# Kernel tuning notes

Measured on AMD Instinct MI355X. Metric: run time of the kernel, lower is better.

## Reference

```python
import jax, jax.numpy as jnp
import numpy as np

BS, NE, NN, CIN, H, D = 8, 4800, 4981, 3, 128, 6
EPG = 19200
NEDGE = BS * EPG
N = BS * NE

PARAM_NAMES = [
    'enc_cw1','enc_cb1','enc_cw2','enc_cb2','enc_cw3','enc_clng','enc_clnb',
    'enc_ew1','enc_eb1','enc_ew2','enc_eb2','enc_ew3','enc_elng','enc_elnb',
    'p_ew1','p_eb1','p_ew2','p_eb2','p_ew3','p_elng','p_elnb',
    'p_nw1','p_nb1','p_nw2','p_nb2','p_nw3','p_nlng','p_nlnb',
    'dec_uw1','dec_ub1','dec_uw2','dec_ub2','dec_uw3','dec_ulng','dec_ulnb',
    'dec_cw1','dec_cb1','dec_cw2','dec_cb2','dec_cw3']


def setup_inputs():
    key = jax.random.key(0)
    ks = iter(jax.random.split(key, 64))
    def nrm(shape, s=0.1):
        return jax.random.normal(next(ks), shape, jnp.float32) * s
    inp = {}
    inp['x'] = jax.random.normal(next(ks), (BS * NN, CIN), jnp.float32)
    inp['elem_conn'] = jax.random.randint(next(ks), (NE, 4), 0, NN)
    inp['edge_index'] = jax.random.randint(next(ks), (2, NEDGE), 0, N)
    inp['enc_cw1'] = nrm((CIN, 4, 1)); inp['enc_cb1'] = nrm((CIN, 1), 0.01)
    inp['enc_cw2'] = nrm((CIN, 1, 1)); inp['enc_cb2'] = nrm((CIN, 1), 0.01)
    inp['enc_cw3'] = nrm((CIN, 1, 1))
    inp['enc_clng'] = jnp.ones((CIN, 1)); inp['enc_clnb'] = jnp.zeros((CIN, 1))
    inp['enc_ew1'] = nrm((CIN, H)); inp['enc_eb1'] = nrm((H,), 0.01)
    inp['enc_ew2'] = nrm((H, H)); inp['enc_eb2'] = nrm((H,), 0.01)
    inp['enc_ew3'] = nrm((H, H))
    inp['enc_elng'] = jnp.ones((H,)); inp['enc_elnb'] = jnp.zeros((H,))
    inp['p_ew1'] = nrm((D, 2 * H, H)); inp['p_eb1'] = nrm((D, H), 0.01)
    inp['p_ew2'] = nrm((D, H, H)); inp['p_eb2'] = nrm((D, H), 0.01)
    inp['p_ew3'] = nrm((D, H, H))
    inp['p_elng'] = jnp.ones((D, H)); inp['p_elnb'] = jnp.zeros((D, H))
    inp['p_nw1'] = nrm((D, 2 * H, H)); inp['p_nb1'] = nrm((D, H), 0.01)
    inp['p_nw2'] = nrm((D, H, H)); inp['p_nb2'] = nrm((D, H), 0.01)
    inp['p_nw3'] = nrm((D, H, H))
    inp['p_nlng'] = jnp.ones((D, H)); inp['p_nlnb'] = jnp.zeros((D, H))
    inp['dec_uw1'] = nrm((H, 1, 4)); inp['dec_ub1'] = nrm((H, 4), 0.01)
    inp['dec_uw2'] = nrm((H, 4, 4)); inp['dec_ub2'] = nrm((H, 4), 0.01)
    inp['dec_uw3'] = nrm((H, 4, 4))
    inp['dec_ulng'] = jnp.ones((H, 4)); inp['dec_ulnb'] = jnp.zeros((H, 4))
    inp['dec_cw1'] = nrm((H, CIN)); inp['dec_cb1'] = nrm((CIN,), 0.01)
    inp['dec_cw2'] = nrm((CIN, CIN)); inp['dec_cb2'] = nrm((CIN,), 0.01)
    inp['dec_cw3'] = nrm((CIN, CIN))
    return inp


def lrelu(x):
    return jnp.where(x >= 0, x, 0.2 * x)


def ln(x, g, b, axis=-1):
    m = jnp.mean(x, axis=axis, keepdims=True)
    v = jnp.var(x, axis=axis, keepdims=True)
    return (x - m) / jnp.sqrt(v + 1e-5) * g + b


def mlp(x, w1, b1, w2, b2, w3):
    h = lrelu(x @ w1 + b1)
    h = lrelu(h @ w2 + b2)
    return h @ w3


def _forward(fl, elem_conn, edge_index):
    x = fl[0]
    P = dict(zip(PARAM_NAMES, fl[1:]))
    # ---- Encoder: MeshCNN gather (4 mesh nodes per element) + per-channel MLP 4->1 ----
    xg = x.reshape(BS, NN, CIN)[:, elem_conn]                  # (BS, NE, 4, CIN)
    h = lrelu(jnp.einsum('beic,cio->beoc', xg, P['enc_cw1']) + P['enc_cb1'].T[None, None])
    h = lrelu(jnp.einsum('beic,cio->beoc', h, P['enc_cw2']) + P['enc_cb2'].T[None, None])
    h = jnp.einsum('beic,cio->beoc', h, P['enc_cw3'])
    h = ln(h, P['enc_clng'].T[None, None], P['enc_clnb'].T[None, None], axis=2)  # LayerNorm(1)
    h = h[:, :, 0, :].reshape(N, CIN)
    h = ln(mlp(h, P['enc_ew1'], P['enc_eb1'], P['enc_ew2'], P['enc_eb2'], P['enc_ew3']),
           P['enc_elng'], P['enc_elnb'])                       # (N, H)
    # ---- Processor: D GraphNet blocks, edge MLP + scatter-add + node MLP ----
    src, dest = edge_index[0], edge_index[1]
    stacked = (P['p_ew1'], P['p_eb1'], P['p_ew2'], P['p_eb2'], P['p_ew3'], P['p_elng'], P['p_elnb'],
               P['p_nw1'], P['p_nb1'], P['p_nw2'], P['p_nb2'], P['p_nw3'], P['p_nlng'], P['p_nlnb'])
    def step(hc, p):
        ew1, eb1, ew2, eb2, ew3, eg, ebv, nw1, nb1, nw2, nb2, nw3, ng, nbv = p
        msg = jnp.concatenate([hc[dest], hc[src]], axis=-1)    # (NEDGE, 2H)
        m = ln(mlp(msg, ew1, eb1, ew2, eb2, ew3), eg, ebv)
        aggr = jax.ops.segment_sum(m, dest, num_segments=N)
        hn = ln(mlp(jnp.concatenate([hc, aggr], axis=-1), nw1, nb1, nw2, nb2, nw3), ng, nbv)
        return hn, None
    h, _ = jax.lax.scan(step, h, stacked)
    # ---- Decoder: per-channel upsample 1->4 then index_add back to mesh nodes ----
    u = h.reshape(BS, NE, H)[:, :, None, :]                    # (BS, NE, 1, H)
    u = lrelu(jnp.einsum('beic,cio->beoc', u, P['dec_uw1']) + P['dec_ub1'].T[None, None])
    u = lrelu(jnp.einsum('beic,cio->beoc', u, P['dec_uw2']) + P['dec_ub2'].T[None, None])
    u = jnp.einsum('beic,cio->beoc', u, P['dec_uw3'])
    u = ln(u, P['dec_ulng'].T[None, None], P['dec_ulnb'].T[None, None], axis=2)  # (BS, NE, 4, H)
    out = jnp.zeros((BS, NN, H), u.dtype).at[:, elem_conn.reshape(-1)].add(u.reshape(BS, NE * 4, H))
    out = out.reshape(BS * NN, H)
    o = lrelu(out @ P['dec_cw1'] + P['dec_cb1'])
    o = lrelu(o @ P['dec_cw2'] + P['dec_cb2'])
    return o @ P['dec_cw3']


def reference(x, elem_conn, edge_index,
              enc_cw1, enc_cb1, enc_cw2, enc_cb2, enc_cw3, enc_clng, enc_clnb,
              enc_ew1, enc_eb1, enc_ew2, enc_eb2, enc_ew3, enc_elng, enc_elnb,
              p_ew1, p_eb1, p_ew2, p_eb2, p_ew3, p_elng, p_elnb,
              p_nw1, p_nb1, p_nw2, p_nb2, p_nw3, p_nlng, p_nlnb,
              dec_uw1, dec_ub1, dec_uw2, dec_ub2, dec_uw3, dec_ulng, dec_ulnb,
              dec_cw1, dec_cb1, dec_cw2, dec_cb2, dec_cw3):
    fl = (x, enc_cw1, enc_cb1, enc_cw2, enc_cb2, enc_cw3, enc_clng, enc_clnb,
          enc_ew1, enc_eb1, enc_ew2, enc_eb2, enc_ew3, enc_elng, enc_elnb,
          p_ew1, p_eb1, p_ew2, p_eb2, p_ew3, p_elng, p_elnb,
          p_nw1, p_nb1, p_nw2, p_nb2, p_nw3, p_nlng, p_nlnb,
          dec_uw1, dec_ub1, dec_uw2, dec_ub2, dec_uw3, dec_ulng, dec_ulnb,
          dec_cw1, dec_cb1, dec_cw2, dec_cb2, dec_cw3)
    return _forward(fl, elem_conn, edge_index)
```

## Files before the change

kernel.cpp:

```cpp
#include <hip/hip_runtime.h>
#include <hip/hip_fp16.h>
#include <math.h>

#define BS    8
#define NE    4800
#define NN    4981
#define CIN   3
#define HD    128
#define DBLK  6
#define NEDGE 153600
#define NTOT  38400
#define NMESH (BS*NN)
#define NNP   5120
#define EM    128
#define TROWS 256

#define UW1T  0
#define UB1T  512
#define UW2T  1024
#define UB2T  3072
#define UW3T  3584
#define ULNGT 5632
#define ULNBT 6144
#define DWT_N 6656

typedef _Float16 f16;
typedef _Float16 f16x8 __attribute__((ext_vector_type(8)));
typedef float f32x4 __attribute__((ext_vector_type(4)));

__device__ __forceinline__ float lrelu(float x) { return x >= 0.0f ? x : 0.2f * x; }

__global__ __launch_bounds__(128)
void enc_msg0_kernel(const float* __restrict__ clnb,
                     const float* __restrict__ ew1, const float* __restrict__ eb1,
                     const float* __restrict__ ew2, const float* __restrict__ eb2,
                     const float* __restrict__ ew3,
                     const float* __restrict__ g, const float* __restrict__ b,
                     float* __restrict__ hv0,
                     const float* __restrict__ pew1, const float* __restrict__ peb1,
                     const float* __restrict__ pew2, const float* __restrict__ peb2,
                     const float* __restrict__ pew3,
                     const float* __restrict__ pg, const float* __restrict__ pb,
                     float* __restrict__ m0) {
    __shared__ float s1[HD], s2[HD], s3[HD], hv[HD];
    int j = threadIdx.x;
    float a = eb1[j];
    for (int c = 0; c < CIN; ++c) a += clnb[c] * ew1[c * HD + j];
    s1[j] = lrelu(a);
    __syncthreads();
    a = eb2[j];
    for (int k = 0; k < HD; ++k) a += s1[k] * ew2[k * HD + j];
    s2[j] = lrelu(a);
    __syncthreads();
    a = 0.0f;
    for (int k = 0; k < HD; ++k) a += s2[k] * ew3[k * HD + j];
    s3[j] = a;
    __syncthreads();
    float m = 0.0f;
    for (int k = 0; k < HD; ++k) m += s3[k];
    m *= (1.0f / HD);
    float v = 0.0f;
    for (int k = 0; k < HD; ++k) { float d = s3[k] - m; v += d * d; }
    v *= (1.0f / HD);
    float rs = 1.0f / sqrtf(v + 1e-5f);
    float h0 = (s3[j] - m) * rs * g[j] + b[j];
    hv0[j] = h0;
    hv[j] = h0;
    __syncthreads();
    a = peb1[j];
    for (int k = 0; k < HD; ++k) a += hv[k] * (pew1[k * HD + j] + pew1[(k + HD) * HD + j]);
    s1[j] = lrelu(a);
    __syncthreads();
    a = peb2[j];
    for (int k = 0; k < HD; ++k) a += s1[k] * pew2[k * HD + j];
    s2[j] = lrelu(a);
    __syncthreads();
    a = 0.0f;
    for (int k = 0; k < HD; ++k) a += s2[k] * pew3[k * HD + j];
    s3[j] = a;
    __syncthreads();
    m = 0.0f;
    for (int k = 0; k < HD; ++k) m += s3[k];
    m *= (1.0f / HD);
    v = 0.0f;
    for (int k = 0; k < HD; ++k) { float d = s3[k] - m; v += d * d; }
    v *= (1.0f / HD);
    rs = 1.0f / sqrtf(v + 1e-5f);
    m0[j] = (s3[j] - m) * rs * pg[j] + pb[j];
}

__global__ __launch_bounds__(256)
void conv_all_kernel(const float* __restrict__ ew1, const float* __restrict__ ew2,
                     const float* __restrict__ ew3,
                     const float* __restrict__ nw1, const float* __restrict__ nw2,
                     const float* __restrict__ nw3, f16* __restrict__ wbuf,
                     const float* __restrict__ eb1, f16* __restrict__ eb16,
                     const float* __restrict__ uw1, const float* __restrict__ ub1,
                     const float* __restrict__ uw2, const float* __restrict__ ub2,
                     const float* __restrict__ uw3, const float* __restrict__ ulng,
                     const float* __restrict__ ulnb, float* __restrict__ dwt,
                     int* __restrict__ degIota) {
    int b = blockIdx.x;
    int tid = threadIdx.x;
    if (b == 48) {
        for (int i = tid; i < DBLK * HD; i += 256)
            eb16[i] = (f16)eb1[i];
        degIota[tid] = tid;
        return;
    }
    if (b == 49) {
        for (int idx = tid; idx < 512; idx += 256) {
            int o = idx >> 7, c = idx & 127;
            dwt[UW1T + idx] = uw1[c * 4 + o];
            dwt[UB1T + idx] = ub1[c * 4 + o];
            dwt[UB2T + idx] = ub2[c * 4 + o];
            dwt[ULNGT + idx] = ulng[c * 4 + o];
            dwt[ULNBT + idx] = ulnb[c * 4 + o];
        }
        for (int idx = tid; idx < 2048; idx += 256) {
            int io = idx >> 7, c = idx & 127;
            dwt[UW2T + idx] = uw2[c * 16 + io];
            dwt[UW3T + idx] = uw3[c * 16 + io];
        }
        return;
    }
    int d = b >> 3, m = b & 7;
    const float* src;
    switch (m) {
        case 0: src = ew1 + (size_t)d * 2 * HD * HD; break;
        case 1: src = ew1 + (size_t)d * 2 * HD * HD + HD * HD; break;
        case 2: src = ew2 + (size_t)d * HD * HD; break;
        case 3: src = ew3 + (size_t)d * HD * HD; break;
        case 4: src = nw1 + (size_t)d * 2 * HD * HD; break;
        case 5: src = nw1 + (size_t)d * 2 * HD * HD + HD * HD; break;
        case 6: src = nw2 + (size_t)d * HD * HD; break;
        default: src = nw3 + (size_t)d * HD * HD; break;
    }
    f16* out = wbuf + (size_t)b * HD * HD;
    for (int idx = tid; idx < HD * HD; idx += 256) {
        int n = idx >> 7, k = idx & 127;
        out[idx] = (f16)src[k * HD + n];
    }
}

#define EHB (NEDGE / 256)
#define MHB (NE * 4 / 256)
#define ESB (NTOT / 256)
#define MSB (NNP / 256)

__global__ __launch_bounds__(256)
void prep_hist(const int* __restrict__ e_dst, const int* __restrict__ conn,
               int* __restrict__ deg, int* __restrict__ mdeg) {
    int b = blockIdx.x;
    if (b < EHB) {
        int e = b * 256 + threadIdx.x;
        atomicAdd(&deg[e_dst[e]], 1);
    } else {
        int idx = (b - EHB) * 256 + threadIdx.x;
        atomicAdd(&mdeg[conn[idx]], 1);
    }
}

__device__ __forceinline__ void scan1_body(const int* __restrict__ deg,
                                           int* __restrict__ rowptr,
                                           int* __restrict__ bsum, int bi) {
    __shared__ int s[256];
    int i = bi * 256 + threadIdx.x;
    int v = deg[i];
    s[threadIdx.x] = v;
    __syncthreads();
    for (int off = 1; off < 256; off <<= 1) {
        int t = (threadIdx.x >= off) ? s[threadIdx.x - off] : 0;
        __syncthreads();
        s[threadIdx.x] += t;
        __syncthreads();
    }
    rowptr[i] = s[threadIdx.x] - v;
    if (threadIdx.x == 255) bsum[bi] = s[255];
}

__global__ __launch_bounds__(256)
void prep_scan1(const int* __restrict__ deg, int* __restrict__ rowptr,
                int* __restrict__ bsum,
                const int* __restrict__ mdeg, int* __restrict__ mrow,
                int* __restrict__ mbsum) {
    int b = blockIdx.x;
    if (b < ESB) scan1_body(deg, rowptr, bsum, b);
    else         scan1_body(mdeg, mrow, mbsum, b - ESB);
}

__device__ __forceinline__ void scan2_body(int* __restrict__ bsum, int nb) {
    __shared__ int s[256];
    int v = (threadIdx.x < nb) ? bsum[threadIdx.x] : 0;
    s[threadIdx.x] = v;
    __syncthreads();
    for (int off = 1; off < 256; off <<= 1) {
        int t = (threadIdx.x >= off) ? s[threadIdx.x - off] : 0;
        __syncthreads();
        s[threadIdx.x] += t;
        __syncthreads();
    }
    if (threadIdx.x < nb) bsum[threadIdx.x] = s[threadIdx.x] - v;
}

__global__ __launch_bounds__(256)
void prep_scan2(int* __restrict__ bsum, int* __restrict__ mbsum) {
    if (blockIdx.x == 0) scan2_body(bsum, ESB);
    else                 scan2_body(mbsum, MSB);
}

__global__ __launch_bounds__(256)
void prep_scan3(int* __restrict__ rowptr, const int* __restrict__ bsum,
                int* __restrict__ mrow, const int* __restrict__ mbsum) {
    int b = blockIdx.x;
    if (b < ESB) {
        int i = b * 256 + threadIdx.x;
        rowptr[i] += bsum[b];
    } else {
        int i = (b - ESB) * 256 + threadIdx.x;
        mrow[i] += mbsum[b - ESB];
    }
}

__global__ __launch_bounds__(256)
void prep_scatter(const int* __restrict__ dest, const int* __restrict__ srcv,
                  const int* __restrict__ rowptr, int* __restrict__ cursor,
                  int* __restrict__ dsorted, int* __restrict__ ssorted,
                  const int* __restrict__ conn, const int* __restrict__ mrow,
                  int* __restrict__ mcur, int* __restrict__ mslot,
                  const int* __restrict__ deg,
                  int* __restrict__ ddegs, int* __restrict__ sdegs) {
    int b = blockIdx.x;
    if (b < EHB) {
        int e = b * 256 + threadIdx.x;
        int d = dest[e];
        int s = srcv[e];
        int pos = rowptr[d] + atomicAdd(&cursor[d], 1);
        dsorted[pos] = d;
        ssorted[pos] = s;
        ddegs[pos] = deg[d];
        sdegs[pos] = deg[s];
    } else {
        int idx = (b - EHB) * 256 + threadIdx.x;
        int nd = conn[idx];
        int pos = mrow[nd] + atomicAdd(&mcur[nd], 1);
        mslot[pos] = idx;
    }
}

template <int NT>
__device__ __forceinline__ void stage_w(const f16* __restrict__ Wg, f16 (*Bt)[HD + 8],
                                        int tid) {
    #pragma unroll
    for (int t = 0; t < 2048 / NT; ++t) {
        int idx = tid + t * NT;
        int r = idx >> 4, c = (idx & 15) * 8;
        *(uint4*)(&Bt[r][c]) = *(const uint4*)(Wg + (size_t)r * HD + c);
    }
}

__device__ __forceinline__ void mfma_pass(const f16 (*A)[HD + 8], const f16 (*Bt)[HD + 8],
                                          int rt_base, int ct_base, int ln, int quad,
                                          f32x4 acc[2][4]) {
    #pragma unroll
    for (int ks = 0; ks < 4; ++ks) {
        int kb = ks * 32 + quad * 8;
        f16x8 a0 = *(const f16x8*)(&A[rt_base + ln][kb]);
        f16x8 a1 = *(const f16x8*)(&A[rt_base + 16 + ln][kb]);
        #pragma unroll
        for (int c = 0; c < 4; ++c) {
            f16x8 b = *(const f16x8*)(&Bt[ct_base + c * 16 + ln][kb]);
            acc[0][c] = __builtin_amdgcn_mfma_f32_16x16x32_f16(a0, b, acc[0][c], 0, 0, 0);
            acc[1][c] = __builtin_amdgcn_mfma_f32_16x16x32_f16(a1, b, acc[1][c], 0, 0, 0);
        }
    }
}

__global__ __launch_bounds__(512, 4)
void gn_edge(const f16* __restrict__ P1, const f16* __restrict__ P2,
             const int* __restrict__ dsorted, const int* __restrict__ ssorted,
             const f16* __restrict__ W2, const f16* __restrict__ W3,
             const f16* __restrict__ b1h, const float* __restrict__ b2,
             const float* __restrict__ g, const float* __restrict__ bln,
             f16* __restrict__ msg) {
    __shared__ __align__(16) f16 As[EM][HD + 8];
    __shared__ __align__(16) f16 Bt[HD][HD + 8];
    __shared__ float red[EM][2][2];

    const int tid = threadIdx.x;
    const int base = blockIdx.x * EM;
    const int wave = tid >> 6, lane = tid & 63;
    const int ln = lane & 15, quad = lane >> 4;
    const int rt_base = (wave >> 1) * 32;
    const int ct_base = (wave & 1) * 64;
    const int half = wave & 1;
    const int r0 = tid >> 4;
    const int cg = (tid & 15) * 8;

    const f16 k02s = (f16)0.2f;
    const f16x8 k02 = {k02s, k02s, k02s, k02s, k02s, k02s, k02s, k02s};

    int dI[4], sI[4];
    #pragma unroll
    for (int it = 0; it < 4; ++it) {
        dI[it] = dsorted[base + r0 + it * 32];
        sI[it] = ssorted[base + r0 + it * 32];
    }
    stage_w<512>(W2, Bt, tid);
    const f16x8 bb = *(const f16x8*)(b1h + cg);
    #pragma unroll
    for (int it = 0; it < 4; ++it) {
        f16x8 p1 = *(const f16x8*)(P1 + (size_t)dI[it] * HD + cg);
        f16x8 p2 = *(const f16x8*)(P2 + (size_t)sI[it] * HD + cg);
        f16x8 s = p1 + p2 + bb;
        *(f16x8*)(&As[r0 + it * 32][cg]) = __builtin_elementwise_max(s, s * k02);
    }
    __syncthreads();

    f32x4 acc[2][4];

    #pragma unroll
    for (int c = 0; c < 4; ++c) {
        float bj = b2[ct_base + c * 16 + ln];
        f32x4 bv = {bj, bj, bj, bj};
        acc[0][c] = bv; acc[1][c] = bv;
    }
    mfma_pass(As, Bt, rt_base, ct_base, ln, quad, acc);
    __syncthreads();
    stage_w<512>(W3, Bt, tid);
    #pragma unroll
    for (int i = 0; i < 2; ++i)
        #pragma unroll
        for (int c = 0; c < 4; ++c)
            #pragma unroll
            for (int r = 0; r < 4; ++r)
                As[rt_base + i * 16 + quad * 4 + r][ct_base + c * 16 + ln] =
                    (f16)lrelu(acc[i][c][r]);
    __syncthreads();

    #pragma unroll
    for (int c = 0; c < 4; ++c) { f32x4 z = {0,0,0,0}; acc[0][c] = z; acc[1][c] = z; }
    mfma_pass(As, Bt, rt_base, ct_base, ln, quad, acc);

    #pragma unroll
    for (int i = 0; i < 2; ++i)
        #pragma unroll
        for (int r = 0; r < 4; ++r) {
            float s = acc[i][0][r] + acc[i][1][r] + acc[i][2][r] + acc[i][3][r];
            float q = acc[i][0][r] * acc[i][0][r] + acc[i][1][r] * acc[i][1][r] +
                      acc[i][2][r] * acc[i][2][r] + acc[i][3][r] * acc[i][3][r];
            s += __shfl_xor(s, 1); q += __shfl_xor(q, 1);
            s += __shfl_xor(s, 2); q += __shfl_xor(q, 2);
            s += __shfl_xor(s, 4); q += __shfl_xor(q, 4);
            s += __shfl_xor(s, 8); q += __shfl_xor(q, 8);
            if (ln == 0) {
                int row = rt_base + i * 16 + quad * 4 + r;
                red[row][half][0] = s;
                red[row][half][1] = q;
            }
        }
    __syncthreads();

    float gv[4], bv[4];
    #pragma unroll
    for (int c = 0; c < 4; ++c) {
        int col = ct_base + c * 16 + ln;
        gv[c] = g[col]; bv[c] = bln[col];
    }
    #pragma unroll
    for (int i = 0; i < 2; ++i)
        #pragma unroll
        for (int r = 0; r < 4; ++r) {
            int row = rt_base + i * 16 + quad * 4 + r;
            float s = red[row][0][0] + red[row][1][0];
            float q = red[row][0][1] + red[row][1][1];
            float m = s * (1.0f / HD);
            float var = q * (1.0f / HD) - m * m;
            float rs = 1.0f / sqrtf(var + 1e-5f);
            #pragma unroll
            for (int c = 0; c < 4; ++c) {
                int col = ct_base + c * 16 + ln;
                float v = (acc[i][c][r] - m) * rs * gv[c] + bv[c];
                msg[(size_t)(base + row) * HD + col] = (f16)v;
            }
        }
}

template <int AGGR, bool PROD, bool DECF, bool HTAB>
__global__ __launch_bounds__(256, 3)
void gn_node(f16* __restrict__ h16, const f16* __restrict__ msg,
             const int* __restrict__ rowptr, const int* __restrict__ deg,
             const float* __restrict__ m0, const float* __restrict__ hv0,
             const f16* __restrict__ htab,
             const f16* __restrict__ W1a, const f16* __restrict__ W1b,
             const f16* __restrict__ W2, const f16* __restrict__ W3,
             const float* __restrict__ b1, const float* __restrict__ b2,
             const float* __restrict__ g, const float* __restrict__ bln,
             const f16* __restrict__ nW1a, const f16* __restrict__ nW1b,
             f16* __restrict__ P1, f16* __restrict__ P2,
             const float* __restrict__ dwt, f16* __restrict__ uval) {
    __shared__ __align__(16) f16 As[64][HD + 8];
    __shared__ __align__(16) f16 Bt[HD][HD + 8];
    __shared__ float red[64][2][2];

    const int tid = threadIdx.x;
    const int base = blockIdx.x * 64;
    const int wave = tid >> 6, lane = tid & 63;
    const int ln = lane & 15, quad = lane >> 4;
    const int rt_base = (wave >> 1) * 32;
    const int ct_base = (wave & 1) * 64;
    const int half = wave & 1;

    f16x8 hreg[4];
    #pragma unroll
    for (int t = 0; t < 4; ++t) {
        int r = (tid >> 4) + t * 16;
        int c = (tid & 15) * 8;
        if (AGGR == 0) {
            f16x8 hz;
            #pragma unroll
            for (int u = 0; u < 8; ++u) hz[u] = (f16)hv0[c + u];
            hreg[t] = hz;
            float sc = (float)deg[base + r];
            f16x8 o;
            #pragma unroll
            for (int u = 0; u < 8; ++u) o[u] = (f16)(sc * m0[c + u]);
            *(f16x8*)(&As[r][c]) = o;
        } else {
            if (HTAB)
                hreg[t] = *(const f16x8*)(htab + (size_t)deg[base + r] * HD + c);
            else
                hreg[t] = *(const f16x8*)(h16 + (size_t)(base + r) * HD + c);
            int rp = rowptr[base + r], dg = deg[base + r];
            float a[8] = {0, 0, 0, 0, 0, 0, 0, 0};
            int j = 0;
            for (; j + 4 <= dg; j += 4) {
                f16x8 v0 = *(const f16x8*)(msg + (size_t)(rp + j) * HD + c);
                f16x8 v1 = *(const f16x8*)(msg + (size_t)(rp + j + 1) * HD + c);
                f16x8 v2 = *(const f16x8*)(msg + (size_t)(rp + j + 2) * HD + c);
                f16x8 v3 = *(const f16x8*)(msg + (size_t)(rp + j + 3) * HD + c);
                #pragma unroll
                for (int u = 0; u < 8; ++u)
                    a[u] += ((float)v0[u] + (float)v1[u]) + ((float)v2[u] + (float)v3[u]);
            }
            for (; j < dg; ++j) {
                f16x8 mv = *(const f16x8*)(msg + (size_t)(rp + j) * HD + c);
                #pragma unroll
                for (int u = 0; u < 8; ++u) a[u] += (float)mv[u];
            }
            f16x8 o;
            #pragma unroll
            for (int u = 0; u < 8; ++u) o[u] = (f16)a[u];
            *(f16x8*)(&As[r][c]) = o;
        }
    }
    stage_w<256>(W1b, Bt, tid);
    __syncthreads();

    f32x4 acc[2][4];
    #pragma unroll
    for (int c = 0; c < 4; ++c) {
        float bj = b1[ct_base + c * 16 + ln];
        f32x4 bb = {bj, bj, bj, bj};
        acc[0][c] = bb; acc[1][c] = bb;
    }
    mfma_pass(As, Bt, rt_base, ct_base, ln, quad, acc);
    __syncthreads();

    #pragma unroll
    for (int t = 0; t < 4; ++t) {
        int r = (tid >> 4) + t * 16;
        int c = (tid & 15) * 8;
        *(f16x8*)(&As[r][c]) = hreg[t];
    }
    stage_w<256>(W1a, Bt, tid);
    __syncthreads();
    mfma_pass(As, Bt, rt_base, ct_base, ln, quad, acc);
    __syncthreads();

    stage_w<256>(W2, Bt, tid);
    #pragma unroll
    for (int i = 0; i < 2; ++i)
        #pragma unroll
        for (int c = 0; c < 4; ++c)
            #pragma unroll
            for (int r = 0; r < 4; ++r)
                As[rt_base + i * 16 + quad * 4 + r][ct_base + c * 16 + ln] =
                    (f16)lrelu(acc[i][c][r]);
    __syncthreads();

    #pragma unroll
    for (int c = 0; c < 4; ++c) {
        float bj = b2[ct_base + c * 16 + ln];
        f32x4 bb = {bj, bj, bj, bj};
        acc[0][c] = bb; acc[1][c] = bb;
    }
    mfma_pass(As, Bt, rt_base, ct_base, ln, quad, acc);
    __syncthreads();
    stage_w<256>(W3, Bt, tid);
    #pragma unroll
    for (int i = 0; i < 2; ++i)
        #pragma unroll
        for (int c = 0; c < 4; ++c)
            #pragma unroll
            for (int r = 0; r < 4; ++r)
                As[rt_base + i * 16 + quad * 4 + r][ct_base + c * 16 + ln] =
                    (f16)lrelu(acc[i][c][r]);
    __syncthreads();

    #pragma unroll
    for (int c = 0; c < 4; ++c) { f32x4 z = {0,0,0,0}; acc[0][c] = z; acc[1][c] = z; }
    mfma_pass(As, Bt, rt_base, ct_base, ln, quad, acc);

    #pragma unroll
    for (int i = 0; i < 2; ++i)
        #pragma unroll
        for (int r = 0; r < 4; ++r) {
            float s = acc[i][0][r] + acc[i][1][r] + acc[i][2][r] + acc[i][3][r];
            float q = acc[i][0][r] * acc[i][0][r] + acc[i][1][r] * acc[i][1][r] +
                      acc[i][2][r] * acc[i][2][r] + acc[i][3][r] * acc[i][3][r];
            s += __shfl_xor(s, 1); q += __shfl_xor(q, 1);
            s += __shfl_xor(s, 2); q += __shfl_xor(q, 2);
            s += __shfl_xor(s, 4); q += __shfl_xor(q, 4);
            s += __shfl_xor(s, 8); q += __shfl_xor(q, 8);
            if (ln == 0) {
                int row = rt_base + i * 16 + quad * 4 + r;
                red[row][half][0] = s;
                red[row][half][1] = q;
            }
        }
    __syncthreads();

    float gv[4], bv[4];
    #pragma unroll
    for (int c = 0; c < 4; ++c) {
        int col = ct_base + c * 16 + ln;
        gv[c] = g[col]; bv[c] = bln[col];
    }

    if (!DECF) {
        #pragma unroll
        for (int i = 0; i < 2; ++i)
            #pragma unroll
            for (int r = 0; r < 4; ++r) {
                int row = rt_base + i * 16 + quad * 4 + r;
                float s = red[row][0][0] + red[row][1][0];
                float q = red[row][0][1] + red[row][1][1];
                float m = s * (1.0f / HD);
                float var = q * (1.0f / HD) - m * m;
                float rs = 1.0f / sqrtf(var + 1e-5f);
                #pragma unroll
                for (int c = 0; c < 4; ++c) {
                    int col = ct_base + c * 16 + ln;
                    float v = (acc[i][c][r] - m) * rs * gv[c] + bv[c];
                    f16 hv = (f16)v;
                    h16[(size_t)(base + row) * HD + col] = hv;
                    if (PROD) As[row][col] = hv;
                }
            }
    } else {
        float mm[2][4], rr[2][4];
        #pragma unroll
        for (int i = 0; i < 2; ++i)
            #pragma unroll
            for (int r = 0; r < 4; ++r) {
                int row = rt_base + i * 16 + quad * 4 + r;
                float s = red[row][0][0] + red[row][1][0];
                float q = red[row][0][1] + red[row][1][1];
                float m = s * (1.0f / HD);
                float var = q * (1.0f / HD) - m * m;
                mm[i][r] = m;
                rr[i][r] = 1.0f / sqrtf(var + 1e-5f);
            }
        #pragma unroll
        for (int c = 0; c < 4; ++c) {
            int col = ct_base + c * 16 + ln;
            float w1v[4], wb1[4], wb2[4], lg4[4], lb4[4];
            #pragma unroll
            for (int o = 0; o < 4; ++o) {
                w1v[o] = dwt[UW1T + o * 128 + col];
                wb1[o] = dwt[UB1T + o * 128 + col];
                wb2[o] = dwt[UB2T + o * 128 + col];
                lg4[o] = dwt[ULNGT + o * 128 + col];
                lb4[o] = dwt[ULNBT + o * 128 + col];
            }
            float w2v[16], w3v[16];
            #pragma unroll
            for (int io = 0; io < 16; ++io) {
                w2v[io] = dwt[UW2T + io * 128 + col];
                w3v[io] = dwt[UW3T + io * 128 + col];
            }
            #pragma unroll
            for (int i = 0; i < 2; ++i)
                #pragma unroll
                for (int r = 0; r < 4; ++r) {
                    int row = rt_base + i * 16 + quad * 4 + r;
                    float v = (acc[i][c][r] - mm[i][r]) * rr[i][r] * gv[c] + bv[c];
                    float s = (float)(f16)v;
                    float u1[4], u2[4], u3[4];
                    #pragma unroll
                    for (int o = 0; o < 4; ++o)
                        u1[o] = lrelu(s * w1v[o] + wb1[o]);
                    #pragma unroll
                    for (int o = 0; o < 4; ++o) {
                        float a = wb2[o];
                        #pragma unroll
                        for (int i2 = 0; i2 < 4; ++i2) a += u1[i2] * w2v[i2 * 4 + o];
                        u2[o] = lrelu(a);
                    }
                    #pragma unroll
                    for (int o = 0; o < 4; ++o) {
                        float a = 0.f;
                        #pragma unroll
                        for (int i2 = 0; i2 < 4; ++i2) a += u2[i2] * w3v[i2 * 4 + o];
                        u3[o] = a;
                    }
                    float m4 = 0.25f * (u3[0] + u3[1] + u3[2] + u3[3]);
                    float var4 = 0.f;
                    #pragma unroll
                    for (int o = 0; o < 4; ++o) { float d = u3[o] - m4; var4 += d * d; }
                    var4 *= 0.25f;
                    float rs4 = 1.0f / sqrtf(var4 + 1e-5f);
                    size_t ub = (size_t)(base + row) * 4 * HD + col;
                    #pragma unroll
                    for (int o = 0; o < 4; ++o)
                        uval[ub + (size_t)o * HD] =
                            (f16)((u3[o] - m4) * rs4 * lg4[o] + lb4[o]);
                }
        }
    }

    if (PROD) {
        __syncthreads();
        stage_w<256>(nW1a, Bt, tid);
        __syncthreads();
        #pragma unroll
        for (int c = 0; c < 4; ++c) { f32x4 z = {0,0,0,0}; acc[0][c] = z; acc[1][c] = z; }
        mfma_pass(As, Bt, rt_base, ct_base, ln, quad, acc);
        #pragma unroll
        for (int i = 0; i < 2; ++i)
            #pragma unroll
            for (int c = 0; c < 4; ++c)
                #pragma unroll
                for (int r = 0; r < 4; ++r)
                    P1[(size_t)(base + rt_base + i * 16 + quad * 4 + r) * HD +
                       ct_base + c * 16 + ln] = (f16)acc[i][c][r];
        __syncthreads();
        stage_w<256>(nW1b, Bt, tid);
        __syncthreads();
        #pragma unroll
        for (int c = 0; c < 4; ++c) { f32x4 z = {0,0,0,0}; acc[0][c] = z; acc[1][c] = z; }
        mfma_pass(As, Bt, rt_base, ct_base, ln, quad, acc);
        #pragma unroll
        for (int i = 0; i < 2; ++i)
            #pragma unroll
            for (int c = 0; c < 4; ++c)
                #pragma unroll
                for (int r = 0; r < 4; ++r)
                    P2[(size_t)(base + rt_base + i * 16 + quad * 4 + r) * HD +
                       ct_base + c * 16 + ln] = (f16)acc[i][c][r];
    }
}

__global__ __launch_bounds__(256)
void dec_gather_out(const f16* __restrict__ uval,
                    const int* __restrict__ mrow, const int* __restrict__ mdeg,
                    const int* __restrict__ mslot,
                    const float* __restrict__ cw1, const float* __restrict__ cb1,
                    const float* __restrict__ cw2, const float* __restrict__ cb2,
                    const float* __restrict__ cw3,
                    float* __restrict__ o, int nrows) {
    int r = blockIdx.x * 4 + (threadIdx.x >> 6);
    if (r >= nrows) return;
    int lane = threadIdx.x & 63;
    int b = r / NN, n = r - b * NN;
    int rp = mrow[n], dg = mdeg[n];
    size_t boff = (size_t)b * NE * 4;
    float a0 = 0.f, a1 = 0.f;
    int j = 0;
    for (; j + 4 <= dg; j += 4) {
        int s0 = mslot[rp + j], s1 = mslot[rp + j + 1];
        int s2 = mslot[rp + j + 2], s3 = mslot[rp + j + 3];
        const f16* u0 = uval + (boff + s0) * HD + lane * 2;
        const f16* u1 = uval + (boff + s1) * HD + lane * 2;
        const f16* u2 = uval + (boff + s2) * HD + lane * 2;
        const f16* u3 = uval + (boff + s3) * HD + lane * 2;
        float b00 = (float)u0[0], b01 = (float)u0[1];
        float b10 = (float)u1[0], b11 = (float)u1[1];
        float b20 = (float)u2[0], b21 = (float)u2[1];
        float b30 = (float)u3[0], b31 = (float)u3[1];
        a0 += (b00 + b10) + (b20 + b30);
        a1 += (b01 + b11) + (b21 + b31);
    }
    for (; j < dg; ++j) {
        int slot = mslot[rp + j];
        const f16* up = uval + (boff + slot) * HD + lane * 2;
        a0 += (float)up[0];
        a1 += (float)up[1];
    }
    int c0 = lane * 2, c1 = lane * 2 + 1;
    float s[3];
    #pragma unroll
    for (int k = 0; k < 3; ++k)
        s[k] = a0 * cw1[c0 * 3 + k] + a1 * cw1[c1 * 3 + k];
    #pragma unroll
    for (int off = 32; off >= 1; off >>= 1) {
        s[0] += __shfl_down(s[0], off);
        s[1] += __shfl_down(s[1], off);
        s[2] += __shfl_down(s[2], off);
    }
    if (lane == 0) {
        float t1[3], t2[3];
        #pragma unroll
        for (int k = 0; k < 3; ++k) t1[k] = lrelu(s[k] + cb1[k]);
        #pragma unroll
        for (int k = 0; k < 3; ++k) {
            float a = cb2[k];
            #pragma unroll
            for (int q = 0; q < 3; ++q) a += t1[q] * cw2[q * 3 + k];
            t2[k] = lrelu(a);
        }
        #pragma unroll
        for (int k = 0; k < 3; ++k) {
            float a = 0.f;
            #pragma unroll
            for (int q = 0; q < 3; ++q) a += t2[q] * cw3[q * 3 + k];
            o[(size_t)r * 3 + k] = a;
        }
    }
}

extern "C" void kernel_launch(void* const* d_in, const int* in_sizes, int n_in,
                              void* d_out, int out_size, void* d_ws, size_t ws_size,
                              hipStream_t stream) {
    const int* elem_conn = (const int*)d_in[1];
    const int* edge_index = (const int*)d_in[2];
    const int* e_src = edge_index;
    const int* e_dst = edge_index + NEDGE;
    const float* enc_clnb = (const float*)d_in[9];
    const float* enc_ew1 = (const float*)d_in[10];
    const float* enc_eb1 = (const float*)d_in[11];
    const float* enc_ew2 = (const float*)d_in[12];
    const float* enc_eb2 = (const float*)d_in[13];
    const float* enc_ew3 = (const float*)d_in[14];
    const float* enc_elng = (const float*)d_in[15];
    const float* enc_elnb = (const float*)d_in[16];
    const float* p_ew1 = (const float*)d_in[17];
    const float* p_eb1 = (const float*)d_in[18];
    const float* p_ew2 = (const float*)d_in[19];
    const float* p_eb2 = (const float*)d_in[20];
    const float* p_ew3 = (const float*)d_in[21];
    const float* p_elng = (const float*)d_in[22];
    const float* p_elnb = (const float*)d_in[23];
    const float* p_nw1 = (const float*)d_in[24];
    const float* p_nb1 = (const float*)d_in[25];
    const float* p_nw2 = (const float*)d_in[26];
    const float* p_nb2 = (const float*)d_in[27];
    const float* p_nw3 = (const float*)d_in[28];
    const float* p_nlng = (const float*)d_in[29];
    const float* p_nlnb = (const float*)d_in[30];
    const float* dec_uw1 = (const float*)d_in[31];
    const float* dec_ub1 = (const float*)d_in[32];
    const float* dec_uw2 = (const float*)d_in[33];
    const float* dec_ub2 = (const float*)d_in[34];
    const float* dec_uw3 = (const float*)d_in[35];
    const float* dec_ulng = (const float*)d_in[36];
    const float* dec_ulnb = (const float*)d_in[37];
    const float* dec_cw1 = (const float*)d_in[38];
    const float* dec_cb1 = (const float*)d_in[39];
    const float* dec_cw2 = (const float*)d_in[40];
    const float* dec_cb2 = (const float*)d_in[41];
    const float* dec_cw3 = (const float*)d_in[42];

    char* ws = (char*)d_ws;
    f16*   h16     = (f16*)(ws);
    f16*   wbuf    = (f16*)(ws + 9830400);
    float* hv0     = (float*)(ws + 11403264);
    float* m0      = (float*)(ws + 11403776);
    f16*   P1      = (f16*)(ws + 11404288);
    f16*   P2      = (f16*)(ws + 21234688);
    f16*   msg     = (f16*)(ws + 31065088);
    int*   deg     = (int*)(ws + 70386688);
    int*   rowptr  = (int*)(ws + 70540288);
    int*   cursor  = (int*)(ws + 70693888);
    int*   bsum    = (int*)(ws + 70847488);
    int*   dsorted = (int*)(ws + 70848512);
    int*   ssorted = (int*)(ws + 71462912);
    f16*   eb16    = (f16*)(ws + 72077312);
    int*   mdeg    = (int*)(ws + 72078848);
    int*   mrow    = (int*)(ws + 72099328);
    int*   mcur    = (int*)(ws + 72119808);
    int*   mbsum   = (int*)(ws + 72140288);
    int*   mslot   = (int*)(ws + 72141312);
    float* dwt     = (float*)(ws + 72218112);
    f16*   uval    = (f16*)(ws + 72244736);
    int*   ddegs   = (int*)(ws + 111566336);
    int*   sdegs   = (int*)(ws + 112180736);
    f16*   tabH    = (f16*)(ws + 112795136);
    f16*   tabP1   = (f16*)(ws + 112860672);
    f16*   tabP2   = (f16*)(ws + 112926208);
    int*   degIota = (int*)(ws + 112991744);

    hipMemsetAsync(deg, 0, 72218112 - 70386688, stream);

    enc_msg0_kernel<<<1, 128, 0, stream>>>(
        enc_clnb, enc_ew1, enc_eb1, enc_ew2, enc_eb2, enc_ew3, enc_elng, enc_elnb, hv0,
        p_ew1, p_eb1, p_ew2, p_eb2, p_ew3, p_elng, p_elnb, m0);
    conv_all_kernel<<<50, 256, 0, stream>>>(p_ew1, p_ew2, p_ew3,
                                            p_nw1, p_nw2, p_nw3, wbuf, p_eb1, eb16,
                                            dec_uw1, dec_ub1, dec_uw2, dec_ub2,
                                            dec_uw3, dec_ulng, dec_ulnb, dwt,
                                            degIota);

    {
        const f16* wd = wbuf;
        const f16* wn = wbuf + (size_t)8 * HD * HD;
        gn_node<0, true, false, false><<<TROWS / 64, 256, 0, stream>>>(
            tabH, nullptr, nullptr, degIota, m0, hv0, nullptr,
            wd + 4 * HD * HD, wd + 5 * HD * HD, wd + 6 * HD * HD, wd + 7 * HD * HD,
            p_nb1, p_nb2, p_nlng, p_nlnb,
            wn + 0 * HD * HD, wn + 1 * HD * HD, tabP1, tabP2, nullptr, nullptr);
    }

    prep_hist<<<EHB + MHB, 256, 0, stream>>>(e_dst, elem_conn, deg, mdeg);
    prep_scan1<<<ESB + MSB, 256, 0, stream>>>(deg, rowptr, bsum, mdeg, mrow, mbsum);
    prep_scan2<<<2, 256, 0, stream>>>(bsum, mbsum);
    prep_scan3<<<ESB + MSB, 256, 0, stream>>>(rowptr, bsum, mrow, mbsum);
    prep_scatter<<<EHB + MHB, 256, 0, stream>>>(e_dst, e_src, rowptr, cursor,
                                                dsorted, ssorted,
                                                elem_conn, mrow, mcur, mslot,
                                                deg, ddegs, sdegs);

    for (int d = 1; d < DBLK; ++d) {
        const f16* wd = wbuf + (size_t)d * 8 * HD * HD;
        if (d == 1)
            gn_edge<<<NEDGE / EM, 512, 0, stream>>>(
                tabP1, tabP2, ddegs, sdegs,
                wd + 2 * HD * HD, wd + 3 * HD * HD,
                eb16 + (size_t)d * HD, p_eb2 + (size_t)d * HD,
                p_elng + (size_t)d * HD, p_elnb + (size_t)d * HD, msg);
        else
            gn_edge<<<NEDGE / EM, 512, 0, stream>>>(
                P1, P2, dsorted, ssorted,
                wd + 2 * HD * HD, wd + 3 * HD * HD,
                eb16 + (size_t)d * HD, p_eb2 + (size_t)d * HD,
                p_elng + (size_t)d * HD, p_elnb + (size_t)d * HD, msg);
        if (d == 1) {
            const f16* wn = wbuf + (size_t)(d + 1) * 8 * HD * HD;
            gn_node<1, true, false, true><<<NTOT / 64, 256, 0, stream>>>(
                h16, msg, rowptr, deg, nullptr, nullptr, tabH,
                wd + 4 * HD * HD, wd + 5 * HD * HD, wd + 6 * HD * HD, wd + 7 * HD * HD,
                p_nb1 + (size_t)d * HD, p_nb2 + (size_t)d * HD,
                p_nlng + (size_t)d * HD, p_nlnb + (size_t)d * HD,
                wn + 0 * HD * HD, wn + 1 * HD * HD, P1, P2, nullptr, nullptr);
        } else if (d < DBLK - 1) {
            const f16* wn = wbuf + (size_t)(d + 1) * 8 * HD * HD;
            gn_node<1, true, false, false><<<NTOT / 64, 256, 0, stream>>>(
                h16, msg, rowptr, deg, nullptr, nullptr, nullptr,
                wd + 4 * HD * HD, wd + 5 * HD * HD, wd + 6 * HD * HD, wd + 7 * HD * HD,
                p_nb1 + (size_t)d * HD, p_nb2 + (size_t)d * HD,
                p_nlng + (size_t)d * HD, p_nlnb + (size_t)d * HD,
                wn + 0 * HD * HD, wn + 1 * HD * HD, P1, P2, nullptr, nullptr);
        } else {
            gn_node<1, false, true, false><<<NTOT / 64, 256, 0, stream>>>(
                h16, msg, rowptr, deg, nullptr, nullptr, nullptr,
                wd + 4 * HD * HD, wd + 5 * HD * HD, wd + 6 * HD * HD, wd + 7 * HD * HD,
                p_nb1 + (size_t)d * HD, p_nb2 + (size_t)d * HD,
                p_nlng + (size_t)d * HD, p_nlnb + (size_t)d * HD,
                wbuf, wbuf, P1, P2, dwt, uval);
        }
    }

    dec_gather_out<<<(NMESH + 3) / 4, 256, 0, stream>>>(
        uval, mrow, mdeg, mslot, dec_cw1, dec_cb1, dec_cw2, dec_cb2, dec_cw3,
        (float*)d_out, NMESH);
}
```

Measured before the change: 564.7 us.

## Fold memset and scan2 into other kernels, pack decoder u-values per channel

```diff
diff --git a/kernel.cpp b/kernel.cpp
--- a/kernel.cpp
+++ b/kernel.cpp
@@ -26,6 +26,7 @@
 
 typedef _Float16 f16;
 typedef _Float16 f16x8 __attribute__((ext_vector_type(8)));
+typedef _Float16 f16x4 __attribute__((ext_vector_type(4)));
 typedef float f32x4 __attribute__((ext_vector_type(4)));
 
 __device__ __forceinline__ float lrelu(float x) { return x >= 0.0f ? x : 0.2f * x; }
@@ -99,7 +100,9 @@
                      const float* __restrict__ uw2, const float* __restrict__ ub2,
                      const float* __restrict__ uw3, const float* __restrict__ ulng,
                      const float* __restrict__ ulnb, float* __restrict__ dwt,
-                     int* __restrict__ degIota) {
+                     int* __restrict__ degIota,
+                     int* __restrict__ zdeg, int* __restrict__ zcur,
+                     int* __restrict__ zmdeg, int* __restrict__ zmcur) {
     int b = blockIdx.x;
     int tid = threadIdx.x;
     if (b == 48) {
@@ -121,6 +124,16 @@
             int io = idx >> 7, c = idx & 127;
             dwt[UW2T + idx] = uw2[c * 16 + io];
             dwt[UW3T + idx] = uw3[c * 16 + io];
+        }
+        return;
+    }
+    if (b >= 50) {
+        uint4 z = {0, 0, 0, 0};
+        for (int idx = (b - 50) * 256 + tid; idx < 21760; idx += 8 * 256) {
+            if (idx < 9600)       ((uint4*)zdeg)[idx] = z;
+            else if (idx < 19200) ((uint4*)zcur)[idx - 9600] = z;
+            else if (idx < 20480) ((uint4*)zmdeg)[idx - 19200] = z;
+            else                  ((uint4*)zmcur)[idx - 20480] = z;
         }
         return;
     }
@@ -189,36 +202,29 @@
     else         scan1_body(mdeg, mrow, mbsum, b - ESB);
 }
 
-__device__ __forceinline__ void scan2_body(int* __restrict__ bsum, int nb) {
-    __shared__ int s[256];
-    int v = (threadIdx.x < nb) ? bsum[threadIdx.x] : 0;
-    s[threadIdx.x] = v;
-    __syncthreads();
-    for (int off = 1; off < 256; off <<= 1) {
-        int t = (threadIdx.x >= off) ? s[threadIdx.x - off] : 0;
-        __syncthreads();
-        s[threadIdx.x] += t;
-        __syncthreads();
-    }
-    if (threadIdx.x < nb) bsum[threadIdx.x] = s[threadIdx.x] - v;
-}
-
-__global__ __launch_bounds__(256)
-void prep_scan2(int* __restrict__ bsum, int* __restrict__ mbsum) {
-    if (blockIdx.x == 0) scan2_body(bsum, ESB);
-    else                 scan2_body(mbsum, MSB);
-}
-
 __global__ __launch_bounds__(256)
 void prep_scan3(int* __restrict__ rowptr, const int* __restrict__ bsum,
                 int* __restrict__ mrow, const int* __restrict__ mbsum) {
+    __shared__ int sb[256];
     int b = blockIdx.x;
+    int tid = threadIdx.x;
     if (b < ESB) {
-        int i = b * 256 + threadIdx.x;
-        rowptr[i] += bsum[b];
+        sb[tid] = (tid < b) ? bsum[tid] : 0;
+        __syncthreads();
+        for (int off = 128; off >= 1; off >>= 1) {
+            if (tid < off) sb[tid] += sb[tid + off];
+            __syncthreads();
+        }
+        rowptr[b * 256 + tid] += sb[0];
     } else {
-        int i = (b - ESB) * 256 + threadIdx.x;
-        mrow[i] += mbsum[b - ESB];
+        int bb = b - ESB;
+        sb[tid] = (tid < bb) ? mbsum[tid] : 0;
+        __syncthreads();
+        for (int off = 128; off >= 1; off >>= 1) {
+            if (tid < off) sb[tid] += sb[tid + off];
+            __syncthreads();
+        }
+        mrow[bb * 256 + tid] += sb[0];
     }
 }
 
@@ -621,11 +627,11 @@
                     for (int o = 0; o < 4; ++o) { float d = u3[o] - m4; var4 += d * d; }
                     var4 *= 0.25f;
                     float rs4 = 1.0f / sqrtf(var4 + 1e-5f);
-                    size_t ub = (size_t)(base + row) * 4 * HD + col;
+                    f16x4 pk;
                     #pragma unroll
                     for (int o = 0; o < 4; ++o)
-                        uval[ub + (size_t)o * HD] =
-                            (f16)((u3[o] - m4) * rs4 * lg4[o] + lb4[o]);
+                        pk[o] = (f16)((u3[o] - m4) * rs4 * lg4[o] + lb4[o]);
+                    *(f16x4*)(uval + ((size_t)(base + row) * HD + col) * 4) = pk;
                 }
         }
     }
@@ -675,30 +681,30 @@
     int lane = threadIdx.x & 63;
     int b = r / NN, n = r - b * NN;
     int rp = mrow[n], dg = mdeg[n];
-    size_t boff = (size_t)b * NE * 4;
+    size_t nbase = (size_t)b * NE;
+    int c0 = lane * 2, c1 = lane * 2 + 1;
     float a0 = 0.f, a1 = 0.f;
     int j = 0;
     for (; j + 4 <= dg; j += 4) {
         int s0 = mslot[rp + j], s1 = mslot[rp + j + 1];
         int s2 = mslot[rp + j + 2], s3 = mslot[rp + j + 3];
-        const f16* u0 = uval + (boff + s0) * HD + lane * 2;
-        const f16* u1 = uval + (boff + s1) * HD + lane * 2;
-        const f16* u2 = uval + (boff + s2) * HD + lane * 2;
-        const f16* u3 = uval + (boff + s3) * HD + lane * 2;
-        float b00 = (float)u0[0], b01 = (float)u0[1];
-        float b10 = (float)u1[0], b11 = (float)u1[1];
-        float b20 = (float)u2[0], b21 = (float)u2[1];
-        float b30 = (float)u3[0], b31 = (float)u3[1];
+        size_t e0 = (nbase + (s0 >> 2)) * (HD * 4) + (s0 & 3);
+        size_t e1 = (nbase + (s1 >> 2)) * (HD * 4) + (s1 & 3);
+        size_t e2 = (nbase + (s2 >> 2)) * (HD * 4) + (s2 & 3);
+        size_t e3 = (nbase + (s3 >> 2)) * (HD * 4) + (s3 & 3);
+        float b00 = (float)uval[e0 + (size_t)c0 * 4], b01 = (float)uval[e0 + (size_t)c1 * 4];
+        float b10 = (float)uval[e1 + (size_t)c0 * 4], b11 = (float)uval[e1 + (size_t)c1 * 4];
+        float b20 = (float)uval[e2 + (size_t)c0 * 4], b21 = (float)uval[e2 + (size_t)c1 * 4];
+        float b30 = (float)uval[e3 + (size_t)c0 * 4], b31 = (float)uval[e3 + (size_t)c1 * 4];
         a0 += (b00 + b10) + (b20 + b30);
         a1 += (b01 + b11) + (b21 + b31);
     }
     for (; j < dg; ++j) {
         int slot = mslot[rp + j];
-        const f16* up = uval + (boff + slot) * HD + lane * 2;
-        a0 += (float)up[0];
-        a1 += (float)up[1];
-    }
-    int c0 = lane * 2, c1 = lane * 2 + 1;
+        size_t eb = (nbase + (slot >> 2)) * (HD * 4) + (slot & 3);
+        a0 += (float)uval[eb + (size_t)c0 * 4];
+        a1 += (float)uval[eb + (size_t)c1 * 4];
+    }
     float s[3];
     #pragma unroll
     for (int k = 0; k < 3; ++k)
@@ -801,16 +807,14 @@
     f16*   tabP2   = (f16*)(ws + 112926208);
     int*   degIota = (int*)(ws + 112991744);
 
-    hipMemsetAsync(deg, 0, 72218112 - 70386688, stream);
-
     enc_msg0_kernel<<<1, 128, 0, stream>>>(
         enc_clnb, enc_ew1, enc_eb1, enc_ew2, enc_eb2, enc_ew3, enc_elng, enc_elnb, hv0,
         p_ew1, p_eb1, p_ew2, p_eb2, p_ew3, p_elng, p_elnb, m0);
-    conv_all_kernel<<<50, 256, 0, stream>>>(p_ew1, p_ew2, p_ew3,
+    conv_all_kernel<<<58, 256, 0, stream>>>(p_ew1, p_ew2, p_ew3,
                                             p_nw1, p_nw2, p_nw3, wbuf, p_eb1, eb16,
                                             dec_uw1, dec_ub1, dec_uw2, dec_ub2,
                                             dec_uw3, dec_ulng, dec_ulnb, dwt,
-                                            degIota);
+                                            degIota, deg, cursor, mdeg, mcur);
 
     {
         const f16* wd = wbuf;
@@ -824,7 +828,6 @@
 
     prep_hist<<<EHB + MHB, 256, 0, stream>>>(e_dst, elem_conn, deg, mdeg);
     prep_scan1<<<ESB + MSB, 256, 0, stream>>>(deg, rowptr, bsum, mdeg, mrow, mbsum);
-    prep_scan2<<<2, 256, 0, stream>>>(bsum, mbsum);
     prep_scan3<<<ESB + MSB, 256, 0, stream>>>(rowptr, bsum, mrow, mbsum);
     prep_scatter<<<EHB + MHB, 256, 0, stream>>>(e_dst, e_src, rowptr, cursor,
                                                 dsorted, ssorted,
```

Result: no change. 569.9 us (+0.9%).
